# Performance work log

Measured on AMD Instinct MI355X. Metric: run time of the kernel, lower is better.

Reference implementation:

```python
import jax, jax.numpy as jnp
import numpy as np
from jax import lax

N_FILTERS = 256
N_ITER = 20
N_HISTORY = 4
N_CLASSES = 100
BITS = 8            # n_bits_activ passed to Quan_layer
POOL_FREQ = 5
EPS = 1e-5


def quantize_ste(w, bits):
    # Uniform symmetric quantization to `bits` with straight-through estimator.
    n = 2.0 ** (bits - 1) - 1.0
    s = jnp.max(jnp.abs(w)) / n
    q = jnp.round(w / s) * s
    return w + lax.stop_gradient(q - w)


def max_pool2(x):
    return lax.reduce_window(x, -jnp.inf, lax.max, (1, 1, 2, 2), (1, 1, 2, 2), 'VALID')


def setup_inputs() -> dict:
    key = jax.random.key(0)
    ks = jax.random.split(key, 5)
    x = jax.random.normal(ks[0], (16, 3, 64, 64), jnp.float32)
    conv_w = jax.random.normal(ks[1], (N_FILTERS, N_FILTERS, 3, 3), jnp.float32) / np.sqrt(9.0 * N_FILTERS).astype(np.float32)
    alpha = jnp.zeros((N_ITER, N_HISTORY + 1), jnp.float32)
    alpha = alpha.at[:, 0].set(0.1).at[:, 1].set(0.9)
    alpha = alpha + 0.01 * jax.random.normal(ks[2], (N_ITER, N_HISTORY + 1), jnp.float32)
    bn_gamma = jnp.ones((N_ITER, N_FILTERS), jnp.float32)
    bn_beta = jnp.zeros((N_ITER, N_FILTERS), jnp.float32)
    out_w = jax.random.normal(ks[3], (N_CLASSES, N_FILTERS), jnp.float32) / np.sqrt(float(N_FILTERS)).astype(np.float32)
    out_b = jnp.zeros((N_CLASSES,), jnp.float32)
    return {'x': x, 'conv_w': conv_w, 'alpha': alpha, 'bn_gamma': bn_gamma,
            'bn_beta': bn_beta, 'out_w': out_w, 'out_b': out_b}


def reference(x, conv_w, alpha, bn_gamma, bn_beta, out_w, out_b):
    pool_at = [t % POOL_FREQ == POOL_FREQ - 1 for t in range(N_ITER)]
    c_in = x.shape[1]
    # zero-pad channels up to n_filters (F.pad on dim 1)
    x = jnp.pad(x, ((0, 0), (0, N_FILTERS - c_in), (0, 0), (0, 0)))
    hist = [None] * (N_HISTORY - 1) + [x]
    wq = quantize_ste(conv_w, BITS)  # shared quantized conv weight
    for t in range(N_ITER):
        a = lax.conv_general_dilated(hist[-1], wq, (1, 1), ((1, 1), (1, 1)),
                                     dimension_numbers=('NCHW', 'OIHW', 'NCHW'))
        a = jax.nn.relu(a)
        a = alpha[t, 0] * a
        for i, h in enumerate(hist):
            if h is not None:
                a = a + alpha[t, i + 1] * h
        # BatchNorm2d (training-mode batch stats, biased variance)
        mean = jnp.mean(a, axis=(0, 2, 3), keepdims=True)
        var = jnp.var(a, axis=(0, 2, 3), keepdims=True)
        a = (a - mean) / jnp.sqrt(var + EPS)
        a = a * bn_gamma[t][None, :, None, None] + bn_beta[t][None, :, None, None]
        # faithful shift: hist[0] is never overwritten (stays None)
        hist = [hist[0]] + hist[2:] + [a]
        if pool_at[t]:
            hist = [None if h is None else max_pool2(h) for h in hist]
    out = jnp.max(hist[-1], axis=(2, 3))  # adaptive_max_pool2d -> (1,1)
    return out @ out_w.T + out_b
```

## Files before the change

kernel.cpp:

```cpp
#include <hip/hip_runtime.h>
#include <hip/hip_fp16.h>
#include <cstddef>
#include <cstdint>


#define NB 16
#define NIT 20

typedef _Float16 half8 __attribute__((ext_vector_type(8)));
typedef _Float16 half4v __attribute__((ext_vector_type(4)));
typedef float floatx4 __attribute__((ext_vector_type(4)));

__device__ __forceinline__ void gl_lds16(const void* g, void* l) {
  __builtin_amdgcn_global_load_lds(
      (const __attribute__((address_space(1))) unsigned int*)g,
      (__attribute__((address_space(3))) unsigned int*)l, 16, 0, 0);
}

__global__ void wmax_part_kernel(const float* __restrict__ w, float* __restrict__ part, int n) {
  float m = 0.f;
  for (int i = blockIdx.x * blockDim.x + threadIdx.x; i < n; i += gridDim.x * blockDim.x)
    m = fmaxf(m, fabsf(w[i]));
  #pragma unroll
  for (int o = 32; o > 0; o >>= 1) m = fmaxf(m, __shfl_down(m, o));
  __shared__ float sm[4];
  int wid = threadIdx.x >> 6, lane = threadIdx.x & 63;
  if (lane == 0) sm[wid] = m;
  __syncthreads();
  if (threadIdx.x == 0) part[blockIdx.x] = fmaxf(fmaxf(sm[0], sm[1]), fmaxf(sm[2], sm[3]));
}

__global__ void wmax_final_kernel(const float* __restrict__ part, float* __restrict__ sout) {
  float m = part[threadIdx.x];
  #pragma unroll
  for (int o = 32; o > 0; o >>= 1) m = fmaxf(m, __shfl_down(m, o));
  __shared__ float sm[4];
  int wid = threadIdx.x >> 6, lane = threadIdx.x & 63;
  if (lane == 0) sm[wid] = m;
  __syncthreads();
  if (threadIdx.x == 0) sout[0] = fmaxf(fmaxf(sm[0], sm[1]), fmaxf(sm[2], sm[3])) / 127.f;
}

__global__ void quant_kernel(const float* __restrict__ w, const float* __restrict__ sptr,
                             _Float16* __restrict__ wqr, int nw) {
  int d = blockIdx.x * 256 + threadIdx.x;
  if (d >= nw) return;
  int frag = d >> 9;
  int e = d & 511;
  int l = e >> 3, j = e & 7;
  int tap = frag >> 7;
  int rem = frag & 127;
  int cog = rem >> 3, chk = rem & 7;
  int co = cog * 16 + (l & 15);
  int ci = chk * 32 + (l >> 4) * 8 + j;
  float s = sptr[0];
  float q = rintf(w[((size_t)co * 256 + ci) * 9 + tap] / s) * s;
  wqr[d] = (_Float16)q;
}

__global__ void pad_kernel(const float* __restrict__ x, _Float16* __restrict__ out) {
  int idx = blockIdx.x * 256 + threadIdx.x;
  int c = idx & 255;
  int pos = idx >> 8;
  int hw = pos & 4095;
  int n = pos >> 12;
  float v = 0.f;
  if (c < 3) v = x[(n * 3 + c) * 4096 + hw];
  out[idx] = (_Float16)v;
}

template <int S, int R, int CO_B, int NWAVES, int MINW>
__global__ __launch_bounds__(NWAVES * 64, MINW) void conv_mfma_v5(
    const _Float16* __restrict__ in, const _Float16* __restrict__ wqr,
    const float* __restrict__ alpha, int t,
    const _Float16* h1, const _Float16* __restrict__ h2,
    const _Float16* __restrict__ h3, _Float16* pre,
    const _Float16* __restrict__ zpage,
    float* __restrict__ psum, float* __restrict__ psum2) {
  constexpr int NT = NWAVES * 64;
  constexpr int LW = S + 2;
  constexpr int XS = (R + 2) * LW * 4;
  constexpr int XS_PAD = ((XS + 63) / 64) * 64;
  constexpr int FRAGS = CO_B / 16;

  __shared__ half8 xl[2][XS_PAD];
  __shared__ half8 wl[2][FRAGS * 64];

  const int tid = threadIdx.x;
  const int lane = tid & 63;
  const int wid = tid >> 6;
  const int l16 = lane & 15;
  const int kg = lane >> 4;
  const int wm = wid >> 2;
  const int wn = wid & 3;

  constexpr int BPI = S / R;
  const int n = blockIdx.x / BPI;
  const int rb = blockIdx.x % BPI;
  const int cob = blockIdx.y * CO_B;

  const _Float16* img = in + (size_t)n * S * S * 256;

  int rg[4], cg[4];
  #pragma unroll
  for (int g = 0; g < 4; ++g) {
    int lp = wn * 64 + g * 16 + l16;
    rg[g] = lp / S;
    cg[g] = lp - rg[g] * S;
  }

  floatx4 acc[4][4];
  #pragma unroll
  for (int f = 0; f < 4; ++f)
    #pragma unroll
    for (int g = 0; g < 4; ++g)
      acc[f][g] = (floatx4){0.f, 0.f, 0.f, 0.f};

  auto stageX = [&](int buf, int c) {
    const _Float16* cbase = img + c * 32;
    for (int sb = wid * 64; sb < XS_PAD; sb += NT) {
      int slot = sb + lane;
      const void* g = (const void*)zpage;
      if (slot < XS) {
        int pix = slot >> 2;
        int cig = (slot & 3) ^ ((pix >> 1) & 3);
        int hp = pix / LW, wp = pix - hp * LW;
        int h = rb * R + hp - 1, w = wp - 1;
        if ((unsigned)h < (unsigned)S && (unsigned)w < (unsigned)S)
          g = (const void*)(cbase + (size_t)(h * S + w) * 256 + cig * 8);
      }
      gl_lds16(g, (void*)&xl[buf][sb]);
    }
  };
  auto stageW = [&](int buf, int c, int tap) {
    const _Float16* g = wqr +
        ((((size_t)tap * 16 + blockIdx.y * FRAGS + wid) * 8 + c) << 9) + lane * 8;
    gl_lds16((const void*)g, (void*)&wl[buf][wid * 64]);
  };

  stageX(0, 0);
  stageW(0, 0, 0);
  __syncthreads();

  for (int s = 0; s < 72; ++s) {
    const int c = s / 9;
    const int tap = s - c * 9;
    if (s < 71) {
      const int s2 = s + 1;
      const int c2 = s2 / 9;
      stageW(s2 & 1, c2, s2 - c2 * 9);
    }
    if (tap == 0 && c < 7) stageX((c + 1) & 1, c + 1);

    const int dh = tap / 3 - 1;
    const int dw = tap - (tap / 3) * 3 - 1;
    const int wbuf = s & 1, xbuf = c & 1;

    half8 af[4];
    #pragma unroll
    for (int f = 0; f < 4; ++f)
      af[f] = wl[wbuf][(wm * 4 + f) * 64 + lane];
    half8 bf[4];
    #pragma unroll
    for (int g = 0; g < 4; ++g) {
      int xp = (rg[g] + 1 + dh) * LW + (cg[g] + 1 + dw);
      bf[g] = xl[xbuf][xp * 4 + (kg ^ ((xp >> 1) & 3))];
    }
    #pragma unroll
    for (int f = 0; f < 4; ++f)
      #pragma unroll
      for (int g = 0; g < 4; ++g)
        acc[f][g] = __builtin_amdgcn_mfma_f32_16x16x32_f16(af[f], bf[g], acc[f][g], 0, 0, 0);
    __syncthreads();
  }

  const float a0 = alpha[t * 5 + 0];
  const float a1 = alpha[t * 5 + 2];
  const float a2 = alpha[t * 5 + 3];
  const float a3 = alpha[t * 5 + 4];
  float ss[4][4], s2v[4][4];
  #pragma unroll
  for (int f = 0; f < 4; ++f)
    #pragma unroll
    for (int r = 0; r < 4; ++r) { ss[f][r] = 0.f; s2v[f][r] = 0.f; }

  const size_t pixbase = (size_t)n * S * S + (size_t)rb * R * S;
  #pragma unroll
  for (int f = 0; f < 4; ++f) {
    const int co = cob + wm * 64 + f * 16 + kg * 4;
    #pragma unroll
    for (int g = 0; g < 4; ++g) {
      int lp = wn * 64 + g * 16 + l16;
      size_t idx = (pixbase + lp) * 256 + co;
      half4v v3 = *(const half4v*)(h3 + idx);
      half4v v1 = {}, v2 = {};
      if (h1) v1 = *(const half4v*)(h1 + idx);
      if (h2) v2 = *(const half4v*)(h2 + idx);
      half4v o;
      #pragma unroll
      for (int r = 0; r < 4; ++r) {
        float pv = a0 * fmaxf(acc[f][g][r], 0.f) + a3 * (float)v3[r];
        if (h1) pv += a1 * (float)v1[r];
        if (h2) pv += a2 * (float)v2[r];
        o[r] = (_Float16)pv;
        ss[f][r] += pv;
        s2v[f][r] += pv * pv;
      }
      *(half4v*)(pre + idx) = o;
    }
  }

  float* sred = (float*)(&wl[0][0]);
  #pragma unroll
  for (int f = 0; f < 4; ++f)
    #pragma unroll
    for (int r = 0; r < 4; ++r) {
      float a = ss[f][r], b = s2v[f][r];
      #pragma unroll
      for (int m = 1; m < 16; m <<= 1) {
        a += __shfl_xor(a, m);
        b += __shfl_xor(b, m);
      }
      if (l16 == 0) {
        sred[wid * 64 + f * 16 + kg * 4 + r] = a;
        sred[NWAVES * 64 + wid * 64 + f * 16 + kg * 4 + r] = b;
      }
    }
  __syncthreads();
  if (tid < CO_B) {
    int half = tid >> 6;
    int ch = tid & 63;
    float a = 0.f, b = 0.f;
    #pragma unroll
    for (int w = 0; w < 4; ++w) {
      a += sred[(half * 4 + w) * 64 + ch];
      b += sred[NWAVES * 64 + (half * 4 + w) * 64 + ch];
    }
    psum[(size_t)blockIdx.x * 256 + cob + tid] = a;
    psum2[(size_t)blockIdx.x * 256 + cob + tid] = b;
  }
}

template <int S, int R>
__global__ __launch_bounds__(512, 2) void conv_mfma_sm(
    const _Float16* __restrict__ in, const _Float16* __restrict__ wqr,
    const float* __restrict__ alpha, int t,
    const _Float16* h1, const _Float16* __restrict__ h2,
    const _Float16* __restrict__ h3, _Float16* pre,
    const _Float16* __restrict__ zpage,
    float* __restrict__ psum, float* __restrict__ psum2) {
  constexpr int LW = S + 2;
  constexpr int PIX = (R + 2) * LW;
  constexpr int XS = PIX * 4;
  constexpr int XS_PAD = ((XS + 63) / 64) * 64;
  constexpr int WS = 36 * 64;
  constexpr int PIXB = R * S;
  constexpr int G = PIXB / 64;

  __shared__ half8 xl[2][XS_PAD];
  __shared__ half8 wl[2][WS];
  __shared__ float sred[8][4][2][4];
  __shared__ float sredq[8][4][2][4];

  const int tid = threadIdx.x;
  const int lane = tid & 63;
  const int wid = tid >> 6;
  const int l16 = lane & 15;
  const int kg = lane >> 4;
  const int wm = wid >> 2;
  const int wn = wid & 3;

  constexpr int BPI = S / R;
  const int n = blockIdx.x / BPI;
  const int rb = blockIdx.x % BPI;
  const int cob = blockIdx.y * 64;

  const _Float16* img = in + (size_t)n * S * S * 256;

  floatx4 acc[2][G];
  #pragma unroll
  for (int f = 0; f < 2; ++f)
    #pragma unroll
    for (int g = 0; g < G; ++g)
      acc[f][g] = (floatx4){0.f, 0.f, 0.f, 0.f};

  auto stage = [&](int buf, int c) {
    const _Float16* cbase = img + c * 32;
    for (int sb = wid * 64; sb < XS_PAD; sb += 512) {
      int slot = sb + lane;
      const void* g = (const void*)zpage;
      if (slot < XS) {
        int pix = slot >> 2;
        int cig = (slot & 3) ^ ((pix >> 1) & 3);
        int hp = pix / LW, wp = pix - hp * LW;
        int h = rb * R + hp - 1, w = wp - 1;
        if ((unsigned)h < (unsigned)S && (unsigned)w < (unsigned)S)
          g = (const void*)(cbase + (size_t)(h * S + w) * 256 + cig * 8);
      }
      gl_lds16(g, (void*)&xl[buf][sb]);
    }
    for (int fb = wid; fb < 36; fb += 8) {
      int tap = fb >> 2, cogl = fb & 3;
      const _Float16* g = wqr +
          ((((size_t)tap * 16 + blockIdx.y * 4 + cogl) * 8 + c) << 9) + lane * 8;
      gl_lds16((const void*)g, (void*)&wl[buf][fb * 64]);
    }
  };

  auto compute = [&](int buf) {
    #pragma unroll
    for (int dh = -1; dh <= 1; ++dh) {
      #pragma unroll
      for (int dw = -1; dw <= 1; ++dw) {
        const int tap = (dh + 1) * 3 + (dw + 1);
        half8 af[2];
        #pragma unroll
        for (int f = 0; f < 2; ++f)
          af[f] = wl[buf][(tap * 4 + wm * 2 + f) * 64 + lane];
        half8 bf[G];
        #pragma unroll
        for (int g = 0; g < G; ++g) {
          int p = wn * (PIXB / 4) + g * 16 + l16;
          int r = p / S, cc = p - r * S;
          int lp = (r + 1 + dh) * LW + (cc + 1 + dw);
          bf[g] = xl[buf][lp * 4 + (kg ^ ((lp >> 1) & 3))];
        }
        #pragma unroll
        for (int f = 0; f < 2; ++f)
          #pragma unroll
          for (int g = 0; g < G; ++g)
            acc[f][g] = __builtin_amdgcn_mfma_f32_16x16x32_f16(af[f], bf[g], acc[f][g], 0, 0, 0);
      }
    }
  };

  stage(0, 0);
  __syncthreads();
  for (int c = 0; c < 8; ++c) {
    if (c < 7) stage((c + 1) & 1, c + 1);
    compute(c & 1);
    __syncthreads();
  }

  const float a0 = alpha[t * 5 + 0];
  const float a1 = alpha[t * 5 + 2];
  const float a2 = alpha[t * 5 + 3];
  const float a3 = alpha[t * 5 + 4];
  float ss[2][4], sq[2][4];
  #pragma unroll
  for (int f = 0; f < 2; ++f)
    #pragma unroll
    for (int r = 0; r < 4; ++r) { ss[f][r] = 0.f; sq[f][r] = 0.f; }

  const size_t pix0 = (size_t)n * S * S + (size_t)rb * PIXB;
  #pragma unroll
  for (int f = 0; f < 2; ++f) {
    const int co = cob + wm * 32 + f * 16 + kg * 4;
    #pragma unroll
    for (int g = 0; g < G; ++g) {
      int p = wn * (PIXB / 4) + g * 16 + l16;
      size_t idx = (pix0 + p) * 256 + co;
      half4v v3 = *(const half4v*)(h3 + idx);
      half4v v1 = {}, v2 = {};
      if (h1) v1 = *(const half4v*)(h1 + idx);
      if (h2) v2 = *(const half4v*)(h2 + idx);
      half4v o;
      #pragma unroll
      for (int r = 0; r < 4; ++r) {
        float pv = a0 * fmaxf(acc[f][g][r], 0.f) + a3 * (float)v3[r];
        if (h1) pv += a1 * (float)v1[r];
        if (h2) pv += a2 * (float)v2[r];
        o[r] = (_Float16)pv;
        ss[f][r] += pv;
        sq[f][r] += pv * pv;
      }
      *(half4v*)(pre + idx) = o;
    }
  }

  #pragma unroll
  for (int f = 0; f < 2; ++f)
    #pragma unroll
    for (int r = 0; r < 4; ++r) {
      float a = ss[f][r], b = sq[f][r];
      #pragma unroll
      for (int m = 1; m < 16; m <<= 1) {
        a += __shfl_xor(a, m);
        b += __shfl_xor(b, m);
      }
      if (l16 == 0) { sred[wid][kg][f][r] = a; sredq[wid][kg][f][r] = b; }
    }
  __syncthreads();
  if (tid < 64) {
    int ch = tid;
    int wmm = ch >> 5, ff = (ch >> 4) & 1, kk = (ch >> 2) & 3, rr = ch & 3;
    float a = 0.f, b = 0.f;
    #pragma unroll
    for (int w = 0; w < 4; ++w) {
      a += sred[wmm * 4 + w][kk][ff][rr];
      b += sredq[wmm * 4 + w][kk][ff][rr];
    }
    psum[(size_t)blockIdx.x * 256 + cob + ch] = a;
    psum2[(size_t)blockIdx.x * 256 + cob + ch] = b;
  }
}

__global__ void stats_final_kernel(const float* __restrict__ psum, const float* __restrict__ psum2,
                                   const float* __restrict__ gamma, const float* __restrict__ beta,
                                   int t, float M, int nblk,
                                   float* __restrict__ scale, float* __restrict__ shift) {
  int c = blockIdx.x;
  float s = 0.f, s2 = 0.f;
  for (int b = threadIdx.x; b < nblk; b += 64) {
    s += psum[(size_t)b * 256 + c];
    s2 += psum2[(size_t)b * 256 + c];
  }
  #pragma unroll
  for (int o = 32; o > 0; o >>= 1) {
    s += __shfl_down(s, o);
    s2 += __shfl_down(s2, o);
  }
  if (threadIdx.x == 0) {
    float mean = s / M;
    float var = s2 / M - mean * mean;
    float sc = gamma[t * 256 + c] * rsqrtf(var + 1e-5f);
    scale[c] = sc;
    shift[c] = beta[t * 256 + c] - mean * sc;
  }
}

__global__ void apply_kernel(_Float16* __restrict__ x, const float* __restrict__ scale,
                             const float* __restrict__ shift, int n8) {
  int i = blockIdx.x * 256 + threadIdx.x;
  if (i >= n8) return;
  half8 v = *(half8*)(x + (size_t)i * 8);
  int c0 = (i * 8) & 255;
  half8 o;
  #pragma unroll
  for (int j = 0; j < 8; ++j) o[j] = (_Float16)((float)v[j] * scale[c0 + j] + shift[c0 + j]);
  *(half8*)(x + (size_t)i * 8) = o;
}

__global__ void pool3_kernel(const _Float16* __restrict__ s0, const _Float16* __restrict__ s1,
                             const _Float16* __restrict__ s2,
                             _Float16* __restrict__ d0, _Float16* __restrict__ d1,
                             _Float16* __restrict__ d2,
                             const float* __restrict__ scale, const float* __restrict__ shift,
                             int So, int total8) {
  int i = blockIdx.x * 256 + threadIdx.x;
  if (i >= total8) return;
  int z = blockIdx.y;
  const _Float16* in = (z == 0) ? s0 : (z == 1) ? s1 : s2;
  _Float16* out = (z == 0) ? d0 : (z == 1) ? d1 : d2;
  int c0 = (i & 31) * 8;
  int pix = i >> 5;
  int wo = pix % So;
  int t1 = pix / So;
  int ho = t1 % So;
  int n = t1 / So;
  int Si = So * 2;
  size_t b00 = ((size_t)(n * Si * Si) + (2 * ho) * Si + 2 * wo) * 256 + c0;
  half8 v00 = *(const half8*)(in + b00);
  half8 v01 = *(const half8*)(in + b00 + 256);
  half8 v10 = *(const half8*)(in + b00 + (size_t)Si * 256);
  half8 v11 = *(const half8*)(in + b00 + (size_t)Si * 256 + 256);
  half8 o;
  if (z == 2) {
    #pragma unroll
    for (int j = 0; j < 8; ++j) {
      float sc = scale[c0 + j], sh = shift[c0 + j];
      float a = (float)v00[j] * sc + sh;
      float b = (float)v01[j] * sc + sh;
      float c = (float)v10[j] * sc + sh;
      float d = (float)v11[j] * sc + sh;
      o[j] = (_Float16)fmaxf(fmaxf(a, b), fmaxf(c, d));
    }
  } else {
    #pragma unroll
    for (int j = 0; j < 8; ++j) {
      float m = fmaxf(fmaxf((float)v00[j], (float)v01[j]),
                      fmaxf((float)v10[j], (float)v11[j]));
      o[j] = (_Float16)m;
    }
  }
  *(half8*)(out + (size_t)pix * 256 + c0) = o;
}

__global__ void amax_kernel(const _Float16* __restrict__ x, float* __restrict__ vec) {
  int i = blockIdx.x * blockDim.x + threadIdx.x;
  if (i >= NB * 256) return;
  int n = i >> 8, c = i & 255;
  float m = -1e30f;
  for (int p = 0; p < 16; ++p)
    m = fmaxf(m, (float)x[((size_t)(n * 16 + p)) * 256 + c]);
  vec[i] = m;
}

__global__ void linear_kernel(const float* __restrict__ vec, const float* __restrict__ W,
                              const float* __restrict__ b, float* __restrict__ out) {
  int n = blockIdx.x, j = threadIdx.x;
  if (j >= 100) return;
  float s = b[j];
  const float* v = vec + n * 256;
  const float* w = W + j * 256;
  for (int c = 0; c < 256; ++c) s += v[c] * w[c];
  out[n * 100 + j] = s;
}

extern "C" void kernel_launch(void* const* d_in, const int* in_sizes, int n_in,
                              void* d_out, int out_size, void* d_ws, size_t ws_size,
                              hipStream_t stream) {
  const float* x        = (const float*)d_in[0];
  const float* conv_w   = (const float*)d_in[1];
  const float* alpha    = (const float*)d_in[2];
  const float* bn_gamma = (const float*)d_in[3];
  const float* bn_beta  = (const float*)d_in[4];
  const float* out_w    = (const float*)d_in[5];
  const float* out_b    = (const float*)d_in[6];
  float* out = (float*)d_out;

  char* ws = (char*)d_ws;
  size_t off = 0;
  auto alloc = [&](size_t bytes) -> void* {
    void* p = (void*)(ws + off);
    off = (off + bytes + 255) & ~(size_t)255;
    return p;
  };
  const size_t SLAB = (size_t)NB * 4096 * 256 * 2;
  char* slab[4];
  size_t slabsz[4];
  for (int i = 0; i < 3; ++i) { slab[i] = (char*)alloc(SLAB); slabsz[i] = SLAB; }
  slab[3] = (char*)alloc(3 * (SLAB / 4)); slabsz[3] = 3 * (SLAB / 4);
  _Float16* wqr  = (_Float16*)alloc((size_t)9 * 256 * 256 * 2);
  float* wpart = (float*)alloc(256 * 4);
  float* sq    = (float*)alloc(256);
  float* psum  = (float*)alloc(256 * 256 * 4);
  float* psum2 = (float*)alloc(256 * 256 * 4);
  float* scale = (float*)alloc(256 * 4);
  float* shift = (float*)alloc(256 * 4);
  float* vec   = (float*)alloc((size_t)NB * 256 * 4);
  _Float16* zpage = (_Float16*)alloc(256);
  (void)ws_size;

  const int NW = 256 * 256 * 9;

  hipMemsetAsync(zpage, 0, 256, stream);

  hipLaunchKernelGGL(wmax_part_kernel, dim3(256), dim3(256), 0, stream, conv_w, wpart, NW);
  hipLaunchKernelGGL(wmax_final_kernel, dim3(1), dim3(256), 0, stream, wpart, sq);
  hipLaunchKernelGGL(quant_kernel, dim3((NW + 255) / 256), dim3(256), 0, stream, conv_w, sq, wqr, NW);

  hipLaunchKernelGGL(pad_kernel, dim3((NB * 4096 * 256) / 256), dim3(256), 0, stream,
                     x, (_Float16*)slab[0]);

  auto contains = [&](int k, char* p) -> bool {
    return p && p >= slab[k] && p < slab[k] + slabsz[k];
  };

  char *p1 = nullptr, *p2 = nullptr, *p3 = slab[0];
  int S = 64;
  for (int t = 0; t < NIT; ++t) {
    char* dst;
    if (p1) {
      dst = p1;
    } else {
      dst = nullptr;
      for (int k = 0; k < 3; ++k)
        if (!contains(k, p2) && !contains(k, p3)) { dst = slab[k]; break; }
    }
    const _Float16* h1 = (const _Float16*)p1;
    const _Float16* h2 = (const _Float16*)p2;
    const _Float16* h3 = (const _Float16*)p3;
    _Float16* pre = (_Float16*)dst;

    int nblk;
    switch (S) {
      case 64: {
        dim3 grid(NB * 16, 2);  nblk = NB * 16;
        hipLaunchKernelGGL((conv_mfma_v5<64, 4, 128, 8, 4>), grid, dim3(512), 0, stream,
                           h3, wqr, alpha, t, h1, h2, h3, pre, zpage, psum, psum2);
        break;
      }
      case 32: {
        dim3 grid(NB * 4, 4);  nblk = NB * 4;
        hipLaunchKernelGGL((conv_mfma_v5<32, 8, 64, 4, 2>), grid, dim3(256), 0, stream,
                           h3, wqr, alpha, t, h1, h2, h3, pre, zpage, psum, psum2);
        break;
      }
      case 16: {
        dim3 grid(NB * 4, 4);  nblk = NB * 4;
        hipLaunchKernelGGL((conv_mfma_sm<16, 4>), grid, dim3(512), 0, stream,
                           h3, wqr, alpha, t, h1, h2, h3, pre, zpage, psum, psum2);
        break;
      }
      default: {
        dim3 grid(NB * 1, 4);  nblk = NB * 1;
        hipLaunchKernelGGL((conv_mfma_sm<8, 8>), grid, dim3(512), 0, stream,
                           h3, wqr, alpha, t, h1, h2, h3, pre, zpage, psum, psum2);
        break;
      }
    }

    int npix = NB * S * S;
    hipLaunchKernelGGL(stats_final_kernel, dim3(256), dim3(64), 0, stream,
                       psum, psum2, bn_gamma, bn_beta, t, (float)npix, nblk, scale, shift);

    if (t % 5 != 4) {
      int n8 = npix * 32;
      hipLaunchKernelGGL(apply_kernel, dim3((n8 + 255) / 256), dim3(256), 0, stream,
                         pre, scale, shift, n8);
      p1 = p2; p2 = p3; p3 = dst;
    } else {
      char* q1 = p2;
      char* q2 = p3;
      char* q3 = dst;
      int So = S / 2;
      size_t qbytes = (size_t)NB * So * So * 256 * 2;
      char* fs = nullptr;
      for (int k = 0; k < 4; ++k)
        if (!contains(k, q1) && !contains(k, q2) && !contains(k, q3)) { fs = slab[k]; break; }
      int total8 = NB * So * So * 32;
      dim3 pg((total8 + 255) / 256, 3);
      hipLaunchKernelGGL(pool3_kernel, pg, dim3(256), 0, stream,
                         (const _Float16*)q1, (const _Float16*)q2, (const _Float16*)q3,
                         (_Float16*)fs, (_Float16*)(fs + qbytes), (_Float16*)(fs + 2 * qbytes),
                         scale, shift, So, total8);
      p1 = fs; p2 = fs + qbytes; p3 = fs + 2 * qbytes;
      S = So;
    }
  }

  hipLaunchKernelGGL(amax_kernel, dim3(16), dim3(256), 0, stream, (const _Float16*)p3, vec);
  hipLaunchKernelGGL(linear_kernel, dim3(NB), dim3(128), 0, stream, vec, out_w, out_b, out);
}
```

Before: 1.203 ms.

## Load conv weight fragments directly to registers and drop per-tap LDS staging

Weight fragments are no longer staged through shared memory each tap. Each wave now loads its A fragments straight from global memory into registers, double-buffered across the nine taps. This leaves one barrier per input-channel chunk instead of one per tap. The cost is more global/L2 weight traffic, since waves no longer share a staged weight tile, plus extra register pressure from the doubled af arrays under a fixed min-4 occupancy bound.

```diff
diff --git a/kernel.cpp b/kernel.cpp
--- a/kernel.cpp
+++ b/kernel.cpp
@@ -69,8 +69,8 @@
   out[idx] = (_Float16)v;
 }
 
-template <int S, int R, int CO_B, int NWAVES, int MINW>
-__global__ __launch_bounds__(NWAVES * 64, MINW) void conv_mfma_v5(
+template <int S, int R, int CO_B, int NWAVES>
+__global__ __launch_bounds__(NWAVES * 64, 4) void conv_mfma_v6(
     const _Float16* __restrict__ in, const _Float16* __restrict__ wqr,
     const float* __restrict__ alpha, int t,
     const _Float16* h1, const _Float16* __restrict__ h2,
@@ -81,17 +81,17 @@
   constexpr int LW = S + 2;
   constexpr int XS = (R + 2) * LW * 4;
   constexpr int XS_PAD = ((XS + 63) / 64) * 64;
-  constexpr int FRAGS = CO_B / 16;
+  static_assert(R * S == 256, "block pixel tile must be 256");
 
   __shared__ half8 xl[2][XS_PAD];
-  __shared__ half8 wl[2][FRAGS * 64];
+  __shared__ float sred[NWAVES * 128];
 
   const int tid = threadIdx.x;
   const int lane = tid & 63;
   const int wid = tid >> 6;
   const int l16 = lane & 15;
   const int kg = lane >> 4;
-  const int wm = wid >> 2;
+  const int wm = (NWAVES == 8) ? (wid >> 2) : 0;
   const int wn = wid & 3;
 
   constexpr int BPI = S / R;
@@ -100,6 +100,8 @@
   const int cob = blockIdx.y * CO_B;
 
   const _Float16* img = in + (size_t)n * S * S * 256;
+  const int cogb = blockIdx.y * (CO_B / 16) + wm * 4;
+  const _Float16* wbase = wqr + (((size_t)cogb * 8) << 9) + lane * 8;
 
   int rg[4], cg[4];
   #pragma unroll
@@ -132,45 +134,41 @@
       gl_lds16(g, (void*)&xl[buf][sb]);
     }
   };
-  auto stageW = [&](int buf, int c, int tap) {
-    const _Float16* g = wqr +
-        ((((size_t)tap * 16 + blockIdx.y * FRAGS + wid) * 8 + c) << 9) + lane * 8;
-    gl_lds16((const void*)g, (void*)&wl[buf][wid * 64]);
-  };
 
   stageX(0, 0);
-  stageW(0, 0, 0);
   __syncthreads();
 
-  for (int s = 0; s < 72; ++s) {
-    const int c = s / 9;
-    const int tap = s - c * 9;
-    if (s < 71) {
-      const int s2 = s + 1;
-      const int c2 = s2 / 9;
-      stageW(s2 & 1, c2, s2 - c2 * 9);
-    }
-    if (tap == 0 && c < 7) stageX((c + 1) & 1, c + 1);
-
-    const int dh = tap / 3 - 1;
-    const int dw = tap - (tap / 3) * 3 - 1;
-    const int wbuf = s & 1, xbuf = c & 1;
-
-    half8 af[4];
+  for (int c = 0; c < 8; ++c) {
+    if (c < 7) stageX((c + 1) & 1, c + 1);
+    const int xbuf = c & 1;
+
+    half8 af[2][4];
     #pragma unroll
     for (int f = 0; f < 4; ++f)
-      af[f] = wl[wbuf][(wm * 4 + f) * 64 + lane];
-    half8 bf[4];
-    #pragma unroll
-    for (int g = 0; g < 4; ++g) {
-      int xp = (rg[g] + 1 + dh) * LW + (cg[g] + 1 + dw);
-      bf[g] = xl[xbuf][xp * 4 + (kg ^ ((xp >> 1) & 3))];
-    }
-    #pragma unroll
-    for (int f = 0; f < 4; ++f)
+      af[0][f] = *(const half8*)(wbase + ((size_t)f * 4096 + (size_t)c * 512));
+
+    #pragma unroll
+    for (int tap = 0; tap < 9; ++tap) {
+      if (tap < 8) {
+        #pragma unroll
+        for (int f = 0; f < 4; ++f)
+          af[(tap + 1) & 1][f] = *(const half8*)(
+              wbase + ((size_t)(tap + 1) * 65536 + (size_t)f * 4096 + (size_t)c * 512));
+      }
+      const int dh = tap / 3 - 1;
+      const int dw = tap - (tap / 3) * 3 - 1;
+      half8 bf[4];
       #pragma unroll
-      for (int g = 0; g < 4; ++g)
-        acc[f][g] = __builtin_amdgcn_mfma_f32_16x16x32_f16(af[f], bf[g], acc[f][g], 0, 0, 0);
+      for (int g = 0; g < 4; ++g) {
+        int xp = (rg[g] + 1 + dh) * LW + (cg[g] + 1 + dw);
+        bf[g] = xl[xbuf][xp * 4 + (kg ^ ((xp >> 1) & 3))];
+      }
+      #pragma unroll
+      for (int f = 0; f < 4; ++f)
+        #pragma unroll
+        for (int g = 0; g < 4; ++g)
+          acc[f][g] = __builtin_amdgcn_mfma_f32_16x16x32_f16(af[tap & 1][f], bf[g], acc[f][g], 0, 0, 0);
+    }
     __syncthreads();
   }
 
@@ -210,7 +208,6 @@
     }
   }
 
-  float* sred = (float*)(&wl[0][0]);
   #pragma unroll
   for (int f = 0; f < 4; ++f)
     #pragma unroll
@@ -577,13 +574,13 @@
     switch (S) {
       case 64: {
         dim3 grid(NB * 16, 2);  nblk = NB * 16;
-        hipLaunchKernelGGL((conv_mfma_v5<64, 4, 128, 8, 4>), grid, dim3(512), 0, stream,
+        hipLaunchKernelGGL((conv_mfma_v6<64, 4, 128, 8>), grid, dim3(512), 0, stream,
                            h3, wqr, alpha, t, h1, h2, h3, pre, zpage, psum, psum2);
         break;
       }
       case 32: {
         dim3 grid(NB * 4, 4);  nblk = NB * 4;
-        hipLaunchKernelGGL((conv_mfma_v5<32, 8, 64, 4, 2>), grid, dim3(256), 0, stream,
+        hipLaunchKernelGGL((conv_mfma_v6<32, 8, 64, 4>), grid, dim3(256), 0, stream,
                            h3, wqr, alpha, t, h1, h2, h3, pre, zpage, psum, psum2);
         break;
       }
```

Result: slower. 1.675 ms (+39.2%).
